# Performance work log

Hardware: AMD Instinct MI355X
Metric: run time of the kernel (lower is better)

Reference implementation:

```python
import jax, jax.numpy as jnp
import numpy as np

N, E, IN, H, C, T = 50000, 800000, 128, 64, 64, 2
F1, FO1 = H, H // T   # conv1: per-tower in/out feats
F2, FO2 = H, C // T   # conv2
STD_EPS = 1e-5
BN_EPS = 1e-5


def setup_inputs() -> dict:
    key = jax.random.key(0)
    ks = jax.random.split(key, 12)
    rn = lambda k, s, sc=0.05: jax.random.normal(k, s, jnp.float32) * sc
    return {
        "x": jax.random.normal(ks[0], (N, IN), jnp.float32),
        "embed_W": rn(ks[1], (IN, H)),
        "embed_b": jnp.zeros((H,), jnp.float32),
        "pre_W1": rn(ks[2], (T, 2 * F1, F1)),
        "pre_b1": jnp.zeros((T, F1), jnp.float32),
        "post_W1": rn(ks[3], (T, 13 * F1, FO1)),
        "post_b1": jnp.zeros((T, FO1), jnp.float32),
        "lin_W1": rn(ks[4], (H, H)),
        "lin_b1": jnp.zeros((H,), jnp.float32),
        "bn_gamma": jnp.ones((H,), jnp.float32),
        "bn_beta": jnp.zeros((H,), jnp.float32),
        "pre_W2": rn(ks[5], (T, 2 * F2, F2)),
        "pre_b2": jnp.zeros((T, F2), jnp.float32),
        "post_W2": rn(ks[6], (T, 13 * F2, FO2)),
        "post_b2": jnp.zeros((T, FO2), jnp.float32),
        "lin_W2": rn(ks[7], (C, C)),
        "lin_b2": jnp.zeros((C,), jnp.float32),
        "src": jax.random.randint(ks[8], (E,), 0, N, jnp.int32),
        "dst": jax.random.randint(ks[9], (E,), 0, N, jnp.int32),
    }


def _pna_conv(h, src, dst, deg_raw, degc, avg_log, preW, preb, postW, postb, linW, linb):
    # h: [N, F] node feats; messages flow src -> dst, aggregated at dst.
    m = jnp.concatenate([h[dst], h[src]], axis=-1)            # [E, 2F]  (cat[x_i, x_j])
    m = jnp.einsum('ef,tfg->etg', m, preW) + preb[None]       # [E, T, F] per-tower pre-NN
    seg = lambda v: jax.ops.segment_sum(v, dst, num_segments=N)
    cnt = degc[:, None, None]                                 # clamped degree >= 1
    has = (deg_raw > 0)[:, None, None]
    mean = seg(m) / cnt                                       # [N, T, F]
    mean_sq = seg(m * m) / cnt
    mn = jnp.where(has, jax.ops.segment_min(m, dst, num_segments=N), 0.0)
    mx = jnp.where(has, jax.ops.segment_max(m, dst, num_segments=N), 0.0)
    std = jnp.sqrt(jax.nn.relu(mean_sq - mean * mean) + STD_EPS)
    agg = jnp.concatenate([mean, mn, mx, std], axis=-1)       # [N, T, 4F]
    ld = jnp.log(degc + 1.0)[:, None, None]
    out = jnp.concatenate([agg, agg * (ld / avg_log), agg * (avg_log / ld)], axis=-1)  # [N, T, 12F]
    F = h.shape[-1]
    out = jnp.concatenate([jnp.broadcast_to(h[:, None, :], (N, T, F)), out], axis=-1)  # [N, T, 13F]
    out = jnp.einsum('ntf,tfg->ntg', out, postW) + postb[None]  # [N, T, FO] per-tower post-NN
    return out.reshape(N, -1) @ linW + linb                    # final mixing Linear(out, out)


def reference(x, embed_W, embed_b, pre_W1, pre_b1, post_W1, post_b1, lin_W1, lin_b1,
              bn_gamma, bn_beta, pre_W2, pre_b2, post_W2, post_b2, lin_W2, lin_b2,
              src, dst):
    deg_raw = jax.ops.segment_sum(jnp.ones((E,), jnp.float32), dst, num_segments=N)
    degc = jnp.maximum(deg_raw, 1.0)
    avg_log = jnp.mean(jnp.log(deg_raw + 1.0))  # avg_deg['log'] from the graph's degrees
    h = x @ embed_W + embed_b
    h = _pna_conv(h, src, dst, deg_raw, degc, avg_log,
                  pre_W1, pre_b1, post_W1, post_b1, lin_W1, lin_b1)
    mu = jnp.mean(h, axis=0)
    var = jnp.mean((h - mu) ** 2, axis=0)
    h = bn_gamma * (h - mu) / jnp.sqrt(var + BN_EPS) + bn_beta
    h = jax.nn.relu(h)  # dropout is identity in eval mode
    return _pna_conv(h, src, dst, deg_raw, degc, avg_log,
                     pre_W2, pre_b2, post_W2, post_b2, lin_W2, lin_b2)
```

## Files before the change

kernel.cpp:

```cpp
#include <hip/hip_runtime.h>
#include <hip/hip_fp16.h>

#define N_NODES 50000
#define E_EDGES 800000
#define IN_F    128
#define H_F     64
#define STD_EPS 1e-5f
#define BN_EPS  1e-5f

#define HIST_BLK 3125
#define EMB_BLK  768
#define SCAN_BLK 49
#define TRANS_BLK 448

typedef __attribute__((ext_vector_type(8))) short bf16x8;
typedef __attribute__((ext_vector_type(4))) float f32x4;

__device__ __forceinline__ unsigned bf16_rne(float f) {
  unsigned u = __float_as_uint(f);
  return (u + 0x7fffu + ((u >> 16) & 1u)) >> 16;
}
__device__ __forceinline__ void bf16_split2(float x, float y, unsigned& hi, unsigned& lo) {
  unsigned hx = bf16_rne(x), hy = bf16_rne(y);
  float rx = x - __uint_as_float(hx << 16);
  float ry = y - __uint_as_float(hy << 16);
  hi = hx | (hy << 16);
  lo = bf16_rne(rx) | (bf16_rne(ry) << 16);
}

#define MFMA(acc, a, b) acc = __builtin_amdgcn_mfma_f32_16x16x32_bf16(a, b, acc, 0, 0, 0)

__global__ __launch_bounds__(256) void k_hist_embed(const int* __restrict__ dst,
                                                    int* __restrict__ deg,
                                                    const float* __restrict__ x,
                                                    const float* __restrict__ W,
                                                    const float* __restrict__ bias,
                                                    float* __restrict__ h) {
  __shared__ float sW[IN_F * 64];
  __shared__ float sx[IN_F * 36];
  if (blockIdx.x < HIST_BLK) {
    int e = blockIdx.x * 256 + threadIdx.x;
    atomicAdd(&deg[dst[e]], 1);
    return;
  }
  for (int i = threadIdx.x; i < IN_F * 64; i += 256) sW[i] = W[i];
  int f = threadIdx.x & 63, ng = threadIdx.x >> 6;
  float bj = bias[f];
  const int NGRP = (N_NODES + 31) / 32;
  for (int grp = blockIdx.x - HIST_BLK; grp < NGRP; grp += EMB_BLK) {
    int n0 = grp * 32;
    __syncthreads();
    for (int idx = threadIdx.x; idx < 32 * IN_F; idx += 256) {
      int nl = idx >> 7, k = idx & 127;
      int n = n0 + nl;
      sx[k * 36 + nl] = (n < N_NODES) ? x[(size_t)n * IN_F + k] : 0.f;
    }
    __syncthreads();
    float a[8] = {bj, bj, bj, bj, bj, bj, bj, bj};
    const float* xp = &sx[ng * 8];
#pragma unroll 4
    for (int k = 0; k < IN_F; k++) {
      float4 h0 = *(const float4*)&xp[k * 36];
      float4 h1 = *(const float4*)&xp[k * 36 + 4];
      float w = sW[k * 64 + f];
      a[0] = fmaf(h0.x, w, a[0]); a[1] = fmaf(h0.y, w, a[1]);
      a[2] = fmaf(h0.z, w, a[2]); a[3] = fmaf(h0.w, w, a[3]);
      a[4] = fmaf(h1.x, w, a[4]); a[5] = fmaf(h1.y, w, a[5]);
      a[6] = fmaf(h1.z, w, a[6]); a[7] = fmaf(h1.w, w, a[7]);
    }
#pragma unroll
    for (int j = 0; j < 8; j++) {
      int n = n0 + ng * 8 + j;
      if (n < N_NODES) h[(size_t)n * 64 + f] = a[j];
    }
  }
}

__global__ __launch_bounds__(256) void k_scanpart_trans(const int* __restrict__ deg,
                                                        int* __restrict__ partials,
                                                        float* __restrict__ scalars,
                                                        const float* __restrict__ pW1,
                                                        const float* __restrict__ pW2,
                                                        const float* __restrict__ lW1,
                                                        const float* __restrict__ lW2,
                                                        unsigned short* __restrict__ WBhi,
                                                        unsigned short* __restrict__ WBlo,
                                                        float* __restrict__ lWT) {
  __shared__ int red[256];
  __shared__ float redf[256];
  if (blockIdx.x < SCAN_BLK) {
    int base = blockIdx.x * 1024;
    int s = 0; float ls = 0.f;
    for (int j = threadIdx.x; j < 1024; j += 256) {
      int i = base + j;
      if (i < N_NODES) { int d = deg[i]; s += d; ls += logf((float)d + 1.0f); }
    }
    red[threadIdx.x] = s; redf[threadIdx.x] = ls; __syncthreads();
    for (int st = 128; st > 0; st >>= 1) {
      if (threadIdx.x < st) {
        red[threadIdx.x] += red[threadIdx.x + st];
        redf[threadIdx.x] += redf[threadIdx.x + st];
      }
      __syncthreads();
    }
    if (threadIdx.x == 0) {
      partials[blockIdx.x] = red[0];
      atomicAdd(&scalars[0], redf[0]);
    }
    return;
  }
  int idx = (blockIdx.x - SCAN_BLK) * 256 + threadIdx.x;
  if (idx < 106496) {
    int f = idx % 832;
    int rest = idx / 832;
    int col = rest & 31, tt = rest >> 5;
    const float* srcp = (tt >= 2) ? pW2 : pW1;
    float v = srcp[((size_t)(tt & 1) * 832 + f) * 32 + col];
    unsigned hb = bf16_rne(v);
    float rsd = v - __uint_as_float(hb << 16);
    WBhi[idx] = (unsigned short)hb;
    WBlo[idx] = (unsigned short)bf16_rne(rsd);
  } else if (idx < 114688) {
    int jj = idx - 106496;
    int layer = jj / 4096, r2 = jj % 4096;
    int c4 = r2 / 256, r3 = r2 % 256;
    int col = r3 / 4, j = r3 % 4;
    const float* srcl = layer ? lW2 : lW1;
    lWT[jj] = srcl[(c4 * 4 + j) * 64 + col];
  }
}

__global__ __launch_bounds__(256) void k_scan_final(const int* __restrict__ deg,
                                                    const int* __restrict__ partials,
                                                    int* __restrict__ row_ptr,
                                                    int* __restrict__ cursor,
                                                    float* __restrict__ scalars) {
  __shared__ int ts[256];
  __shared__ int sbase;
  if (threadIdx.x == 0) {
    int pre = 0;
    for (int b = 0; b < (int)blockIdx.x; b++) pre += partials[b];
    sbase = pre;
    if (blockIdx.x == 0) {
      scalars[1] = scalars[0] / (float)N_NODES;
      row_ptr[N_NODES] = E_EDGES;
    }
  }
  int base = blockIdx.x * 1024 + threadIdx.x * 4;
  int d[4]; int s = 0;
#pragma unroll
  for (int j = 0; j < 4; j++) {
    int i = base + j;
    d[j] = (i < N_NODES) ? deg[i] : 0;
    s += d[j];
  }
  ts[threadIdx.x] = s; __syncthreads();
  for (int off = 1; off < 256; off <<= 1) {
    int t = (threadIdx.x >= off) ? ts[threadIdx.x - off] : 0;
    __syncthreads();
    ts[threadIdx.x] += t;
    __syncthreads();
  }
  int excl = (threadIdx.x > 0) ? ts[threadIdx.x - 1] : 0;
  int run = sbase + excl;
#pragma unroll
  for (int j = 0; j < 4; j++) {
    int i = base + j;
    if (i < N_NODES) { row_ptr[i] = run; cursor[i] = run; run += d[j]; }
  }
}

__global__ __launch_bounds__(256) void k_scatter(const int* __restrict__ src,
                                                 const int* __restrict__ dst,
                                                 int* __restrict__ cursor,
                                                 int* __restrict__ csr_src) {
  int e = blockIdx.x * 256 + threadIdx.x;
  if (e < E_EDGES) {
    int d = dst[e];
    int p = atomicAdd(&cursor[d], 1);
    csr_src[p] = src[e];
  }
}

template <bool BN>
__global__ __launch_bounds__(256) void k_preab(const float* __restrict__ hin,
                                               const float* __restrict__ preW,
                                               const float* __restrict__ preb,
                                               const float* __restrict__ bnsum,
                                               const float* __restrict__ bnsumsq,
                                               const float* __restrict__ gamma,
                                               const float* __restrict__ beta,
                                               float* __restrict__ h2out,
                                               float* __restrict__ hA,
                                               __half* __restrict__ hB) {
  __shared__ float sWp[64 * 128];
  __shared__ float sh[64 * 68];
  __shared__ float sbn[128];
  int t = blockIdx.x & 1;
  const float* Wsrc = preW + (size_t)t * 128 * 64;
  for (int i = threadIdx.x; i < 64 * 64; i += 256) {
    int k = i >> 6, f = i & 63;
    float wa = Wsrc[k * 64 + f];
    float wb = Wsrc[(64 + k) * 64 + f];
    *(float2*)&sWp[k * 128 + f * 2] = make_float2(wa, wb);
  }
  if (BN && threadIdx.x < 64) {
    int c = threadIdx.x;
    float mu = bnsum[c] * (1.f / N_NODES);
    float var = bnsumsq[c] * (1.f / N_NODES) - mu * mu;
    float sc = gamma[c] / sqrtf(var + BN_EPS);
    sbn[c] = sc;
    sbn[64 + c] = fmaf(-mu, sc, beta[c]);
  }
  int f = threadIdx.x & 63, ng = threadIdx.x >> 6;
  float pb = preb[t * 64 + f];
  int nblk2 = gridDim.x >> 1;
  const int NGRP = (N_NODES + 63) / 64;
  for (int grp = blockIdx.x >> 1; grp < NGRP; grp += nblk2) {
    int n0 = grp * 64;
    __syncthreads();
    for (int idx = threadIdx.x; idx < 64 * 64; idx += 256) {
      int nl = idx >> 6, k = idx & 63;
      int n = n0 + nl;
      float v = 0.f;
      if (n < N_NODES) {
        v = hin[(size_t)n * 64 + k];
        if (BN) {
          v = fmaxf(fmaf(v, sbn[k], sbn[64 + k]), 0.f);
          if (t == 0) h2out[(size_t)n * 64 + k] = v;
        }
      }
      sh[k * 68 + nl] = v;
    }
    __syncthreads();
    float a[16], b[16];
#pragma unroll
    for (int j = 0; j < 16; j++) { a[j] = pb; b[j] = 0.f; }
    const float* hp = &sh[ng * 16];
    const float* wp = &sWp[f * 2];
#pragma unroll 2
    for (int k = 0; k < 64; k++) {
      float4 h0 = *(const float4*)&hp[k * 68];
      float4 h1 = *(const float4*)&hp[k * 68 + 4];
      float4 h2 = *(const float4*)&hp[k * 68 + 8];
      float4 h3 = *(const float4*)&hp[k * 68 + 12];
      float2 w2 = *(const float2*)&wp[k * 128];
      a[0]  = fmaf(h0.x, w2.x, a[0]);  b[0]  = fmaf(h0.x, w2.y, b[0]);
      a[1]  = fmaf(h0.y, w2.x, a[1]);  b[1]  = fmaf(h0.y, w2.y, b[1]);
      a[2]  = fmaf(h0.z, w2.x, a[2]);  b[2]  = fmaf(h0.z, w2.y, b[2]);
      a[3]  = fmaf(h0.w, w2.x, a[3]);  b[3]  = fmaf(h0.w, w2.y, b[3]);
      a[4]  = fmaf(h1.x, w2.x, a[4]);  b[4]  = fmaf(h1.x, w2.y, b[4]);
      a[5]  = fmaf(h1.y, w2.x, a[5]);  b[5]  = fmaf(h1.y, w2.y, b[5]);
      a[6]  = fmaf(h1.z, w2.x, a[6]);  b[6]  = fmaf(h1.z, w2.y, b[6]);
      a[7]  = fmaf(h1.w, w2.x, a[7]);  b[7]  = fmaf(h1.w, w2.y, b[7]);
      a[8]  = fmaf(h2.x, w2.x, a[8]);  b[8]  = fmaf(h2.x, w2.y, b[8]);
      a[9]  = fmaf(h2.y, w2.x, a[9]);  b[9]  = fmaf(h2.y, w2.y, b[9]);
      a[10] = fmaf(h2.z, w2.x, a[10]); b[10] = fmaf(h2.z, w2.y, b[10]);
      a[11] = fmaf(h2.w, w2.x, a[11]); b[11] = fmaf(h2.w, w2.y, b[11]);
      a[12] = fmaf(h3.x, w2.x, a[12]); b[12] = fmaf(h3.x, w2.y, b[12]);
      a[13] = fmaf(h3.y, w2.x, a[13]); b[13] = fmaf(h3.y, w2.y, b[13]);
      a[14] = fmaf(h3.z, w2.x, a[14]); b[14] = fmaf(h3.z, w2.y, b[14]);
      a[15] = fmaf(h3.w, w2.x, a[15]); b[15] = fmaf(h3.w, w2.y, b[15]);
    }
    int tf = t * 64 + f;
#pragma unroll
    for (int j = 0; j < 16; j++) {
      int n = n0 + ng * 16 + j;
      if (n < N_NODES) {
        hA[(size_t)n * 128 + tf] = a[j];
        hB[(size_t)n * 128 + tf] = __float2half(b[j]);
      }
    }
  }
}

__global__ __launch_bounds__(256, 8) void k_conv(const float* __restrict__ hA,
                                                 const __half* __restrict__ hB,
                                                 const float* __restrict__ hskip,
                                                 const int* __restrict__ row_ptr,
                                                 const int* __restrict__ csr_src,
                                                 const unsigned short* __restrict__ WBhi,
                                                 const unsigned short* __restrict__ WBlo,
                                                 const float* __restrict__ postb,
                                                 const float* __restrict__ linWT,
                                                 const float* __restrict__ linb,
                                                 const float* __restrict__ scalars,
                                                 float* __restrict__ out) {
  __shared__ unsigned sAhi[2560];
  __shared__ unsigned sAlo[2560];
  int w = threadIdx.x >> 6, lane = threadIdx.x & 63;
  int n0 = blockIdx.x * 8;
  int t = lane >> 5, fb2 = (lane & 31) * 2;
  int off = t * 64 + fb2;
  float avg = scalars[1];

#pragma unroll 1
  for (int k = 0; k < 2; k++) {
    int nl = w * 2 + k;
    int n = n0 + nl;
    float2 a = *(const float2*)&hA[(size_t)n * 128 + off];
    float2 hsv = *(const float2*)&hskip[(size_t)n * 64 + fb2];
    int rp0 = __builtin_amdgcn_readfirstlane(row_ptr[n]);
    int rp1 = __builtin_amdgcn_readfirstlane(row_ptr[n + 1]);
    int dg = rp1 - rp0;
    float sx0=0,sy0=0,qx0=0,qy0=0, sx1=0,sy1=0,qx1=0,qy1=0;
    float mnx0=INFINITY,mny0=INFINITY,mxx0=-INFINITY,mxy0=-INFINITY;
    float mnx1=INFINITY,mny1=INFINITY,mxx1=-INFINITY,mxy1=-INFINITY;
    int nloop = dg >> 3;
    if (nloop > 0) {
      int b = rp0;
      int s0=csr_src[b],s1=csr_src[b+1],s2=csr_src[b+2],s3=csr_src[b+3],
          s4=csr_src[b+4],s5=csr_src[b+5],s6=csr_src[b+6],s7=csr_src[b+7];
      __half2 qa0 = *(const __half2*)&hB[(size_t)s0 * 128 + off];
      __half2 qa1 = *(const __half2*)&hB[(size_t)s1 * 128 + off];
      __half2 qa2 = *(const __half2*)&hB[(size_t)s2 * 128 + off];
      __half2 qa3 = *(const __half2*)&hB[(size_t)s3 * 128 + off];
      __half2 qa4 = *(const __half2*)&hB[(size_t)s4 * 128 + off];
      __half2 qa5 = *(const __half2*)&hB[(size_t)s5 * 128 + off];
      __half2 qa6 = *(const __half2*)&hB[(size_t)s6 * 128 + off];
      __half2 qa7 = *(const __half2*)&hB[(size_t)s7 * 128 + off];
      for (int it = 0; ; it++) {
        bool more = (it + 1 < nloop);
        __half2 qb0, qb1, qb2, qb3, qb4, qb5, qb6, qb7;
        if (more) {
          int c = rp0 + ((it + 1) << 3);
          s0=csr_src[c];s1=csr_src[c+1];s2=csr_src[c+2];s3=csr_src[c+3];
          s4=csr_src[c+4];s5=csr_src[c+5];s6=csr_src[c+6];s7=csr_src[c+7];
          qb0 = *(const __half2*)&hB[(size_t)s0 * 128 + off];
          qb1 = *(const __half2*)&hB[(size_t)s1 * 128 + off];
          qb2 = *(const __half2*)&hB[(size_t)s2 * 128 + off];
          qb3 = *(const __half2*)&hB[(size_t)s3 * 128 + off];
          qb4 = *(const __half2*)&hB[(size_t)s4 * 128 + off];
          qb5 = *(const __half2*)&hB[(size_t)s5 * 128 + off];
          qb6 = *(const __half2*)&hB[(size_t)s6 * 128 + off];
          qb7 = *(const __half2*)&hB[(size_t)s7 * 128 + off];
        }
        float2 v0 = __half22float2(qa0), v1 = __half22float2(qa1);
        float2 v2 = __half22float2(qa2), v3 = __half22float2(qa3);
        float2 v4 = __half22float2(qa4), v5 = __half22float2(qa5);
        float2 v6 = __half22float2(qa6), v7 = __half22float2(qa7);
        sx0 += v0.x; qx0 = fmaf(v0.x,v0.x,qx0); mnx0 = fminf(mnx0,v0.x); mxx0 = fmaxf(mxx0,v0.x);
        sy0 += v0.y; qy0 = fmaf(v0.y,v0.y,qy0); mny0 = fminf(mny0,v0.y); mxy0 = fmaxf(mxy0,v0.y);
        sx1 += v1.x; qx1 = fmaf(v1.x,v1.x,qx1); mnx1 = fminf(mnx1,v1.x); mxx1 = fmaxf(mxx1,v1.x);
        sy1 += v1.y; qy1 = fmaf(v1.y,v1.y,qy1); mny1 = fminf(mny1,v1.y); mxy1 = fmaxf(mxy1,v1.y);
        sx0 += v2.x; qx0 = fmaf(v2.x,v2.x,qx0); mnx0 = fminf(mnx0,v2.x); mxx0 = fmaxf(mxx0,v2.x);
        sy0 += v2.y; qy0 = fmaf(v2.y,v2.y,qy0); mny0 = fminf(mny0,v2.y); mxy0 = fmaxf(mxy0,v2.y);
        sx1 += v3.x; qx1 = fmaf(v3.x,v3.x,qx1); mnx1 = fminf(mnx1,v3.x); mxx1 = fmaxf(mxx1,v3.x);
        sy1 += v3.y; qy1 = fmaf(v3.y,v3.y,qy1); mny1 = fminf(mny1,v3.y); mxy1 = fmaxf(mxy1,v3.y);
        sx0 += v4.x; qx0 = fmaf(v4.x,v4.x,qx0); mnx0 = fminf(mnx0,v4.x); mxx0 = fmaxf(mxx0,v4.x);
        sy0 += v4.y; qy0 = fmaf(v4.y,v4.y,qy0); mny0 = fminf(mny0,v4.y); mxy0 = fmaxf(mxy0,v4.y);
        sx1 += v5.x; qx1 = fmaf(v5.x,v5.x,qx1); mnx1 = fminf(mnx1,v5.x); mxx1 = fmaxf(mxx1,v5.x);
        sy1 += v5.y; qy1 = fmaf(v5.y,v5.y,qy1); mny1 = fminf(mny1,v5.y); mxy1 = fmaxf(mxy1,v5.y);
        sx0 += v6.x; qx0 = fmaf(v6.x,v6.x,qx0); mnx0 = fminf(mnx0,v6.x); mxx0 = fmaxf(mxx0,v6.x);
        sy0 += v6.y; qy0 = fmaf(v6.y,v6.y,qy0); mny0 = fminf(mny0,v6.y); mxy0 = fmaxf(mxy0,v6.y);
        sx1 += v7.x; qx1 = fmaf(v7.x,v7.x,qx1); mnx1 = fminf(mnx1,v7.x); mxx1 = fmaxf(mxx1,v7.x);
        sy1 += v7.y; qy1 = fmaf(v7.y,v7.y,qy1); mny1 = fminf(mny1,v7.y); mxy1 = fmaxf(mxy1,v7.y);
        if (!more) break;
        qa0=qb0; qa1=qb1; qa2=qb2; qa3=qb3; qa4=qb4; qa5=qb5; qa6=qb6; qa7=qb7;
      }
    }
    {
      int i = rp0 + (nloop << 3);
      int r = rp1 - i;
      if (r > 0) {
        int sj[7];
#pragma unroll
        for (int j = 0; j < 7; j++) sj[j] = csr_src[i + (j < r ? j : r - 1)];
        __half2 hq[7];
#pragma unroll
        for (int j = 0; j < 7; j++) hq[j] = *(const __half2*)&hB[(size_t)sj[j] * 128 + off];
#pragma unroll
        for (int j = 0; j < 7; j++) {
          if (j < r) {
            float2 v = __half22float2(hq[j]);
            if (j & 1) {
              sx1 += v.x; qx1 = fmaf(v.x,v.x,qx1); mnx1 = fminf(mnx1,v.x); mxx1 = fmaxf(mxx1,v.x);
              sy1 += v.y; qy1 = fmaf(v.y,v.y,qy1); mny1 = fminf(mny1,v.y); mxy1 = fmaxf(mxy1,v.y);
            } else {
              sx0 += v.x; qx0 = fmaf(v.x,v.x,qx0); mnx0 = fminf(mnx0,v.x); mxx0 = fmaxf(mxx0,v.x);
              sy0 += v.y; qy0 = fmaf(v.y,v.y,qy0); mny0 = fminf(mny0,v.y); mxy0 = fmaxf(mxy0,v.y);
            }
          }
        }
      }
    }
    float cnt = (float)(dg > 0 ? dg : 1);
    float inv = 1.0f / cnt;
    float mrx = (sx0 + sx1) * inv, mry = (sy0 + sy1) * inv;
    float sdx = sqrtf(fmaxf((qx0 + qx1) * inv - mrx * mrx, 0.f) + STD_EPS);
    float sdy = sqrtf(fmaxf((qy0 + qy1) * inv - mry * mry, 0.f) + STD_EPS);
    float mnx = fminf(mnx0, mnx1), mny = fminf(mny0, mny1);
    float mxx = fmaxf(mxx0, mxx1), mxy = fmaxf(mxy0, mxy1);
    float ax = a.x, ay = a.y;
    if (dg == 0) { mnx = 0; mny = 0; mxx = 0; mxy = 0; ax = 0; ay = 0; }
    float meanx = mrx + ax, meany = mry + ay;
    mnx += ax; mny += ay; mxx += ax; mxy += ay;
    unsigned* ahp = &sAhi[(t * 8 + nl) * 160];
    unsigned* alp = &sAlo[(t * 8 + nl) * 160];
    int sw = (nl & 3) << 2;
    int p = lane & 31;
    unsigned hi, lo;
    bf16_split2(hsv.x, hsv.y, hi, lo);   ahp[p ^ sw]         = hi; alp[p ^ sw]         = lo;
    bf16_split2(meanx, meany, hi, lo);   ahp[(p + 32) ^ sw]  = hi; alp[(p + 32) ^ sw]  = lo;
    bf16_split2(mnx, mny, hi, lo);       ahp[(p + 64) ^ sw]  = hi; alp[(p + 64) ^ sw]  = lo;
    bf16_split2(mxx, mxy, hi, lo);       ahp[(p + 96) ^ sw]  = hi; alp[(p + 96) ^ sw]  = lo;
    bf16_split2(sdx, sdy, hi, lo);       ahp[(p + 128) ^ sw] = hi; alp[(p + 128) ^ sw] = lo;
  }
  __syncthreads();

  f32x4 acc1 = {0.f, 0.f, 0.f, 0.f};
  f32x4 acc2 = {0.f, 0.f, 0.f, 0.f};
  f32x4 acc3 = {0.f, 0.f, 0.f, 0.f};
  int tw = w >> 1, ntile = w & 1;
  int kq = lane >> 4;
  {
    const bf16x8* Ah = (const bf16x8*)(sAhi + (tw * 8 + (lane & 7)) * 160);
    const bf16x8* Al = (const bf16x8*)(sAlo + (tw * 8 + (lane & 7)) * 160);
    int kqs = kq ^ (lane & 3);
    int brow = (tw * 32 + ntile * 16 + (lane & 15)) * 104 + kq;
    const bf16x8* Bh = (const bf16x8*)WBhi + brow;
    const bf16x8* Bl = (const bf16x8*)WBlo + brow;
    bf16x8 bh_0 = Bh[0], bl_0 = Bl[0];
    bf16x8 bh_1 = Bh[4], bl_1 = Bl[4];
#pragma unroll
    for (int s = 0; s < 10; s++) {
      bf16x8 bh_n, bl_n;
      if (s < 8) { bh_n = Bh[(s + 2) * 4]; bl_n = Bl[(s + 2) * 4]; }
      bf16x8 ah = Ah[s * 4 + kqs], al = Al[s * 4 + kqs];
      MFMA(acc1, ah, bh_0); MFMA(acc1, al, bh_0); MFMA(acc1, ah, bl_0);
      bh_0 = bh_1; bl_0 = bl_1; bh_1 = bh_n; bl_1 = bl_n;
    }
    bf16x8 c_0 = Bh[40], d_0 = Bh[72];
    bf16x8 c_1 = Bh[44], d_1 = Bh[76];
#pragma unroll
    for (int s = 0; s < 8; s++) {
      bf16x8 c_n, d_n;
      if (s < 6) { c_n = Bh[48 + s * 4]; d_n = Bh[80 + s * 4]; }
      bf16x8 ah = Ah[(s + 2) * 4 + kqs], al = Al[(s + 2) * 4 + kqs];
      MFMA(acc2, ah, c_0); MFMA(acc2, al, c_0);
      MFMA(acc3, ah, d_0); MFMA(acc3, al, d_0);
      c_0 = c_1; d_0 = d_1; c_1 = c_n; d_1 = d_n;
    }
  }
  __syncthreads();

  float* spo = (float*)sAhi;
  if (lane < 32) {
    int colg = tw * 32 + ntile * 16 + (lane & 15);
    float pbv = postb[colg];
    int rbase = kq * 4;
    int rb = n0 + rbase;
    int p0 = row_ptr[rb], p1 = row_ptr[rb+1], p2 = row_ptr[rb+2],
        p3 = row_ptr[rb+3], p4 = row_ptr[rb+4];
    int dgv[4] = {p1 - p0, p2 - p1, p3 - p2, p4 - p3};
#pragma unroll
    for (int r = 0; r < 4; r++) {
      float cnt = (float)(dgv[r] > 0 ? dgv[r] : 1);
      float ldv = logf(cnt + 1.f);
      spo[(rbase + r) * 64 + colg] =
          acc1[r] + (ldv / avg) * acc2[r] + (avg / ldv) * acc3[r] + pbv;
    }
  }
  __syncthreads();

  {
    float la0 = linb[lane], la1 = la0;
    const float4* lw4 = (const float4*)linWT + lane;
    const float* p0 = &spo[(w * 2) * 64];
    const float* p1 = p0 + 64;
#pragma unroll
    for (int c4 = 0; c4 < 16; c4++) {
      float4 lwv = lw4[c4 * 64];
      float4 pa = *(const float4*)&p0[c4 * 4];
      float4 pb2 = *(const float4*)&p1[c4 * 4];
      la0 = fmaf(pa.w, lwv.w, fmaf(pa.z, lwv.z, fmaf(pa.y, lwv.y, fmaf(pa.x, lwv.x, la0))));
      la1 = fmaf(pb2.w, lwv.w, fmaf(pb2.z, lwv.z, fmaf(pb2.y, lwv.y, fmaf(pb2.x, lwv.x, la1))));
    }
    size_t ob = (size_t)(n0 + w * 2) * 64 + lane;
    out[ob] = la0;
    out[ob + 64] = la1;
  }
}

__global__ __launch_bounds__(256) void k_bnstats(const float* __restrict__ y,
                                                 float* __restrict__ bnsum,
                                                 float* __restrict__ bnsumsq) {
  __shared__ float r1[256], r2[256];
  int c = threadIdx.x & 63, r = threadIdx.x >> 6;
  float s = 0, q = 0;
  for (int n = blockIdx.x * 4 + r; n < N_NODES; n += gridDim.x * 4) {
    float v = y[(size_t)n * 64 + c];
    s += v; q = fmaf(v, v, q);
  }
  r1[threadIdx.x] = s; r2[threadIdx.x] = q; __syncthreads();
  if (threadIdx.x < 64) {
    s = r1[threadIdx.x] + r1[threadIdx.x + 64] + r1[threadIdx.x + 128] + r1[threadIdx.x + 192];
    q = r2[threadIdx.x] + r2[threadIdx.x + 64] + r2[threadIdx.x + 128] + r2[threadIdx.x + 192];
    atomicAdd(&bnsum[threadIdx.x], s);
    atomicAdd(&bnsumsq[threadIdx.x], q);
  }
}

extern "C" void kernel_launch(void* const* d_in, const int* in_sizes, int n_in,
                              void* d_out, int out_size, void* d_ws, size_t ws_size,
                              hipStream_t stream) {
  const float* x      = (const float*)d_in[0];
  const float* embW   = (const float*)d_in[1];
  const float* embB   = (const float*)d_in[2];
  const float* preW1  = (const float*)d_in[3];
  const float* preb1  = (const float*)d_in[4];
  const float* postW1 = (const float*)d_in[5];
  const float* postb1 = (const float*)d_in[6];
  const float* linW1  = (const float*)d_in[7];
  const float* linb1  = (const float*)d_in[8];
  const float* gamma  = (const float*)d_in[9];
  const float* beta   = (const float*)d_in[10];
  const float* preW2  = (const float*)d_in[11];
  const float* preb2  = (const float*)d_in[12];
  const float* postW2 = (const float*)d_in[13];
  const float* postb2 = (const float*)d_in[14];
  const float* linW2  = (const float*)d_in[15];
  const float* linb2  = (const float*)d_in[16];
  const int*   src    = (const int*)d_in[17];
  const int*   dst    = (const int*)d_in[18];
  float* out = (float*)d_out;

  char* w = (char*)d_ws;
  size_t o = 0;
  int*   deg     = (int*)(w + o);   o += (size_t)N_NODES * 4;
  float* scalars = (float*)(w + o); o += 64;
  float* bnsum   = (float*)(w + o); o += 256;
  float* bnsumsq = (float*)(w + o); o += 256;
  size_t zero_len = o;
  o = (o + 255) & ~(size_t)255;
  int* partials = (int*)(w + o);  o += 256;
  int* row_ptr  = (int*)(w + o);  o += (size_t)(N_NODES + 1) * 4; o = (o + 255) & ~(size_t)255;
  int* cursor   = (int*)(w + o);  o += (size_t)N_NODES * 4;       o = (o + 255) & ~(size_t)255;
  int* csr      = (int*)(w + o);  o += (size_t)E_EDGES * 4;       o = (o + 255) & ~(size_t)255;
  unsigned short* WBhi = (unsigned short*)(w + o); o += (size_t)2 * 53248 * 2;
  unsigned short* WBlo = (unsigned short*)(w + o); o += (size_t)2 * 53248 * 2;
  float* linWT  = (float*)(w + o); o += (size_t)2 * 4096 * 4;
  float* h1 = (float*)(w + o); o += (size_t)N_NODES * 64 * 4;
  float* y1 = (float*)(w + o); o += (size_t)N_NODES * 64 * 4;
  float* h2 = (float*)(w + o); o += (size_t)N_NODES * 64 * 4;
  float* hA = (float*)(w + o); o += (size_t)N_NODES * 128 * 4;
  __half* hBh = (__half*)(w + o); o += (size_t)N_NODES * 128 * 2;

  hipMemsetAsync(w, 0, zero_len, stream);

  k_hist_embed<<<HIST_BLK + EMB_BLK, 256, 0, stream>>>(dst, deg, x, embW, embB, h1);
  k_scanpart_trans<<<SCAN_BLK + TRANS_BLK, 256, 0, stream>>>(
      deg, partials, scalars, postW1, postW2, linW1, linW2, WBhi, WBlo, linWT);
  k_scan_final<<<SCAN_BLK, 256, 0, stream>>>(deg, partials, row_ptr, cursor, scalars);
  k_scatter<<<(E_EDGES + 255) / 256, 256, 0, stream>>>(src, dst, cursor, csr);

  k_preab<false><<<768, 256, 0, stream>>>(h1, preW1, preb1, nullptr, nullptr,
                                          nullptr, nullptr, nullptr, hA, hBh);
  k_conv<<<N_NODES / 8, 256, 0, stream>>>(hA, hBh, h1, row_ptr, csr,
                                          WBhi, WBlo, postb1, linWT, linb1, scalars, y1);
  k_bnstats<<<256, 256, 0, stream>>>(y1, bnsum, bnsumsq);
  k_preab<true><<<768, 256, 0, stream>>>(y1, preW2, preb2, bnsum, bnsumsq,
                                         gamma, beta, h2, hA, hBh);
  k_conv<<<N_NODES / 8, 256, 0, stream>>>(hA, hBh, h2, row_ptr, csr,
                                          WBhi + 53248, WBlo + 53248, postb2,
                                          linWT + 4096, linb2, scalars, out);
}
```

Measured before the change: 574.9 us.

## Interleave gather loops for two nodes per wave with padded 8-edge batches

Each wave now gathers neighbours for both of its nodes together, with double-buffered 8-edge batches for each node, instead of processing the two nodes one after the other. The tail is handled by clamping indices and masking, so the separate remainder path is gone. Edge indices are made wave-uniform with readfirstlane, and the LDS swizzle is widened from 4 to 8 rows to cut bank conflicts. The cost is more registers, so launch bounds drop from 8 to 6 blocks per CU, and padded batches issue redundant loads.

```diff
diff --git a/kernel.cpp b/kernel.cpp
--- a/kernel.cpp
+++ b/kernel.cpp
@@ -274,7 +274,65 @@
   }
 }
 
-__global__ __launch_bounds__(256, 8) void k_conv(const float* __restrict__ hA,
+#define GATHER8(D0,D1,D2,D3,D4,D5,D6,D7, bb, rl)                              \
+  { int _s0 = __builtin_amdgcn_readfirstlane(csr_src[min((bb)+0,(rl))]);      \
+    int _s1 = __builtin_amdgcn_readfirstlane(csr_src[min((bb)+1,(rl))]);      \
+    int _s2 = __builtin_amdgcn_readfirstlane(csr_src[min((bb)+2,(rl))]);      \
+    int _s3 = __builtin_amdgcn_readfirstlane(csr_src[min((bb)+3,(rl))]);      \
+    int _s4 = __builtin_amdgcn_readfirstlane(csr_src[min((bb)+4,(rl))]);      \
+    int _s5 = __builtin_amdgcn_readfirstlane(csr_src[min((bb)+5,(rl))]);      \
+    int _s6 = __builtin_amdgcn_readfirstlane(csr_src[min((bb)+6,(rl))]);      \
+    int _s7 = __builtin_amdgcn_readfirstlane(csr_src[min((bb)+7,(rl))]);      \
+    D0 = hB2[((size_t)_s0 << 6) + oh2];                                       \
+    D1 = hB2[((size_t)_s1 << 6) + oh2];                                       \
+    D2 = hB2[((size_t)_s2 << 6) + oh2];                                       \
+    D3 = hB2[((size_t)_s3 << 6) + oh2];                                       \
+    D4 = hB2[((size_t)_s4 << 6) + oh2];                                       \
+    D5 = hB2[((size_t)_s5 << 6) + oh2];                                       \
+    D6 = hB2[((size_t)_s6 << 6) + oh2];                                       \
+    D7 = hB2[((size_t)_s7 << 6) + oh2]; }
+
+#define EDGE1(vv, P, S)                                                       \
+  { float2 _f = __half22float2(vv);                                           \
+    P##sx##S += _f.x; P##qx##S = fmaf(_f.x, _f.x, P##qx##S);                  \
+    P##mnx##S = fminf(P##mnx##S, _f.x); P##mxx##S = fmaxf(P##mxx##S, _f.x);   \
+    P##sy##S += _f.y; P##qy##S = fmaf(_f.y, _f.y, P##qy##S);                  \
+    P##mny##S = fminf(P##mny##S, _f.y); P##mxy##S = fmaxf(P##mxy##S, _f.y); }
+
+#define COMP8(A0,A1,A2,A3,A4,A5,A6,A7, m8, dg, P)                             \
+  { if ((m8)+0 < (dg)) EDGE1(A0, P, 0);                                       \
+    if ((m8)+1 < (dg)) EDGE1(A1, P, 1);                                       \
+    if ((m8)+2 < (dg)) EDGE1(A2, P, 0);                                       \
+    if ((m8)+3 < (dg)) EDGE1(A3, P, 1);                                       \
+    if ((m8)+4 < (dg)) EDGE1(A4, P, 0);                                       \
+    if ((m8)+5 < (dg)) EDGE1(A5, P, 1);                                       \
+    if ((m8)+6 < (dg)) EDGE1(A6, P, 0);                                       \
+    if ((m8)+7 < (dg)) EDGE1(A7, P, 1); }
+
+#define FINALIZE(P, dg, a, hs, nl)                                            \
+  { float cnt = (float)((dg) > 0 ? (dg) : 1);                                 \
+    float inv = 1.0f / cnt;                                                   \
+    float mrx = (P##sx0 + P##sx1) * inv, mry = (P##sy0 + P##sy1) * inv;       \
+    float sdx = sqrtf(fmaxf((P##qx0 + P##qx1) * inv - mrx * mrx, 0.f) + STD_EPS); \
+    float sdy = sqrtf(fmaxf((P##qy0 + P##qy1) * inv - mry * mry, 0.f) + STD_EPS); \
+    float mnx = fminf(P##mnx0, P##mnx1), mny = fminf(P##mny0, P##mny1);       \
+    float mxx = fmaxf(P##mxx0, P##mxx1), mxy = fmaxf(P##mxy0, P##mxy1);       \
+    float ax = (a).x, ay = (a).y;                                             \
+    if ((dg) == 0) { mnx = 0; mny = 0; mxx = 0; mxy = 0; ax = 0; ay = 0; }    \
+    float meanx = mrx + ax, meany = mry + ay;                                 \
+    mnx += ax; mny += ay; mxx += ax; mxy += ay;                               \
+    unsigned* ahp = &sAhi[(t * 8 + (nl)) * 160];                              \
+    unsigned* alp = &sAlo[(t * 8 + (nl)) * 160];                              \
+    int sw = ((nl) & 7) << 2;                                                 \
+    int p = lane & 31;                                                        \
+    unsigned hi, lo;                                                          \
+    bf16_split2((hs).x, (hs).y, hi, lo); ahp[p ^ sw] = hi; alp[p ^ sw] = lo;  \
+    bf16_split2(meanx, meany, hi, lo); ahp[(p+32) ^ sw] = hi; alp[(p+32) ^ sw] = lo; \
+    bf16_split2(mnx, mny, hi, lo);     ahp[(p+64) ^ sw] = hi; alp[(p+64) ^ sw] = lo; \
+    bf16_split2(mxx, mxy, hi, lo);     ahp[(p+96) ^ sw] = hi; alp[(p+96) ^ sw] = lo; \
+    bf16_split2(sdx, sdy, hi, lo);     ahp[(p+128) ^ sw] = hi; alp[(p+128) ^ sw] = lo; }
+
+__global__ __launch_bounds__(256, 6) void k_conv(const float* __restrict__ hA,
                                                  const __half* __restrict__ hB,
                                                  const float* __restrict__ hskip,
                                                  const int* __restrict__ row_ptr,
@@ -294,118 +352,50 @@
   int off = t * 64 + fb2;
   float avg = scalars[1];
 
+  const __half2* hB2 = (const __half2*)hB;
+  int oh2 = (t << 5) | (lane & 31);
+
+  int nu = n0 + w * 2;
+  float2 au = *(const float2*)&hA[(size_t)nu * 128 + off];
+  float2 av = *(const float2*)&hA[(size_t)(nu + 1) * 128 + off];
+  float2 hsu = *(const float2*)&hskip[(size_t)nu * 64 + fb2];
+  float2 hsv = *(const float2*)&hskip[(size_t)(nu + 1) * 64 + fb2];
+  int rpu0 = __builtin_amdgcn_readfirstlane(row_ptr[nu]);
+  int rpu1 = __builtin_amdgcn_readfirstlane(row_ptr[nu + 1]);
+  int rpv1 = __builtin_amdgcn_readfirstlane(row_ptr[nu + 2]);
+  int dgu = rpu1 - rpu0, dgv = rpv1 - rpu1;
+  int rlu = rpu1 - 1, rlv = rpv1 - 1;
+  int nbu = (dgu + 7) >> 3, nbv = (dgv + 7) >> 3;
+  int M = nbu > nbv ? nbu : nbv;
+
+  float usx0=0,uqx0=0,usy0=0,uqy0=0, usx1=0,uqx1=0,usy1=0,uqy1=0;
+  float umnx0=INFINITY,umny0=INFINITY,umxx0=-INFINITY,umxy0=-INFINITY;
+  float umnx1=INFINITY,umny1=INFINITY,umxx1=-INFINITY,umxy1=-INFINITY;
+  float vsx0=0,vqx0=0,vsy0=0,vqy0=0, vsx1=0,vqx1=0,vsy1=0,vqy1=0;
+  float vmnx0=INFINITY,vmny0=INFINITY,vmxx0=-INFINITY,vmxy0=-INFINITY;
+  float vmnx1=INFINITY,vmny1=INFINITY,vmxx1=-INFINITY,vmxy1=-INFINITY;
+
+  __half2 UA0{},UA1{},UA2{},UA3{},UA4{},UA5{},UA6{},UA7{};
+  __half2 UB0{},UB1{},UB2{},UB3{},UB4{},UB5{},UB6{},UB7{};
+  __half2 VA0{},VA1{},VA2{},VA3{},VA4{},VA5{},VA6{},VA7{};
+  __half2 VB0{},VB1{},VB2{},VB3{},VB4{},VB5{},VB6{},VB7{};
+
+  if (nbu > 0) GATHER8(UA0,UA1,UA2,UA3,UA4,UA5,UA6,UA7, rpu0, rlu);
+  if (nbv > 0) GATHER8(VA0,VA1,VA2,VA3,VA4,VA5,VA6,VA7, rpu1, rlv);
 #pragma unroll 1
-  for (int k = 0; k < 2; k++) {
-    int nl = w * 2 + k;
-    int n = n0 + nl;
-    float2 a = *(const float2*)&hA[(size_t)n * 128 + off];
-    float2 hsv = *(const float2*)&hskip[(size_t)n * 64 + fb2];
-    int rp0 = __builtin_amdgcn_readfirstlane(row_ptr[n]);
-    int rp1 = __builtin_amdgcn_readfirstlane(row_ptr[n + 1]);
-    int dg = rp1 - rp0;
-    float sx0=0,sy0=0,qx0=0,qy0=0, sx1=0,sy1=0,qx1=0,qy1=0;
-    float mnx0=INFINITY,mny0=INFINITY,mxx0=-INFINITY,mxy0=-INFINITY;
-    float mnx1=INFINITY,mny1=INFINITY,mxx1=-INFINITY,mxy1=-INFINITY;
-    int nloop = dg >> 3;
-    if (nloop > 0) {
-      int b = rp0;
-      int s0=csr_src[b],s1=csr_src[b+1],s2=csr_src[b+2],s3=csr_src[b+3],
-          s4=csr_src[b+4],s5=csr_src[b+5],s6=csr_src[b+6],s7=csr_src[b+7];
-      __half2 qa0 = *(const __half2*)&hB[(size_t)s0 * 128 + off];
-      __half2 qa1 = *(const __half2*)&hB[(size_t)s1 * 128 + off];
-      __half2 qa2 = *(const __half2*)&hB[(size_t)s2 * 128 + off];
-      __half2 qa3 = *(const __half2*)&hB[(size_t)s3 * 128 + off];
-      __half2 qa4 = *(const __half2*)&hB[(size_t)s4 * 128 + off];
-      __half2 qa5 = *(const __half2*)&hB[(size_t)s5 * 128 + off];
-      __half2 qa6 = *(const __half2*)&hB[(size_t)s6 * 128 + off];
-      __half2 qa7 = *(const __half2*)&hB[(size_t)s7 * 128 + off];
-      for (int it = 0; ; it++) {
-        bool more = (it + 1 < nloop);
-        __half2 qb0, qb1, qb2, qb3, qb4, qb5, qb6, qb7;
-        if (more) {
-          int c = rp0 + ((it + 1) << 3);
-          s0=csr_src[c];s1=csr_src[c+1];s2=csr_src[c+2];s3=csr_src[c+3];
-          s4=csr_src[c+4];s5=csr_src[c+5];s6=csr_src[c+6];s7=csr_src[c+7];
-          qb0 = *(const __half2*)&hB[(size_t)s0 * 128 + off];
-          qb1 = *(const __half2*)&hB[(size_t)s1 * 128 + off];
-          qb2 = *(const __half2*)&hB[(size_t)s2 * 128 + off];
-          qb3 = *(const __half2*)&hB[(size_t)s3 * 128 + off];
-          qb4 = *(const __half2*)&hB[(size_t)s4 * 128 + off];
-          qb5 = *(const __half2*)&hB[(size_t)s5 * 128 + off];
-          qb6 = *(const __half2*)&hB[(size_t)s6 * 128 + off];
-          qb7 = *(const __half2*)&hB[(size_t)s7 * 128 + off];
-        }
-        float2 v0 = __half22float2(qa0), v1 = __half22float2(qa1);
-        float2 v2 = __half22float2(qa2), v3 = __half22float2(qa3);
-        float2 v4 = __half22float2(qa4), v5 = __half22float2(qa5);
-        float2 v6 = __half22float2(qa6), v7 = __half22float2(qa7);
-        sx0 += v0.x; qx0 = fmaf(v0.x,v0.x,qx0); mnx0 = fminf(mnx0,v0.x); mxx0 = fmaxf(mxx0,v0.x);
-        sy0 += v0.y; qy0 = fmaf(v0.y,v0.y,qy0); mny0 = fminf(mny0,v0.y); mxy0 = fmaxf(mxy0,v0.y);
-        sx1 += v1.x; qx1 = fmaf(v1.x,v1.x,qx1); mnx1 = fminf(mnx1,v1.x); mxx1 = fmaxf(mxx1,v1.x);
-        sy1 += v1.y; qy1 = fmaf(v1.y,v1.y,qy1); mny1 = fminf(mny1,v1.y); mxy1 = fmaxf(mxy1,v1.y);
-        sx0 += v2.x; qx0 = fmaf(v2.x,v2.x,qx0); mnx0 = fminf(mnx0,v2.x); mxx0 = fmaxf(mxx0,v2.x);
-        sy0 += v2.y; qy0 = fmaf(v2.y,v2.y,qy0); mny0 = fminf(mny0,v2.y); mxy0 = fmaxf(mxy0,v2.y);
-        sx1 += v3.x; qx1 = fmaf(v3.x,v3.x,qx1); mnx1 = fminf(mnx1,v3.x); mxx1 = fmaxf(mxx1,v3.x);
-        sy1 += v3.y; qy1 = fmaf(v3.y,v3.y,qy1); mny1 = fminf(mny1,v3.y); mxy1 = fmaxf(mxy1,v3.y);
-        sx0 += v4.x; qx0 = fmaf(v4.x,v4.x,qx0); mnx0 = fminf(mnx0,v4.x); mxx0 = fmaxf(mxx0,v4.x);
-        sy0 += v4.y; qy0 = fmaf(v4.y,v4.y,qy0); mny0 = fminf(mny0,v4.y); mxy0 = fmaxf(mxy0,v4.y);
-        sx1 += v5.x; qx1 = fmaf(v5.x,v5.x,qx1); mnx1 = fminf(mnx1,v5.x); mxx1 = fmaxf(mxx1,v5.x);
-        sy1 += v5.y; qy1 = fmaf(v5.y,v5.y,qy1); mny1 = fminf(mny1,v5.y); mxy1 = fmaxf(mxy1,v5.y);
-        sx0 += v6.x; qx0 = fmaf(v6.x,v6.x,qx0); mnx0 = fminf(mnx0,v6.x); mxx0 = fmaxf(mxx0,v6.x);
-        sy0 += v6.y; qy0 = fmaf(v6.y,v6.y,qy0); mny0 = fminf(mny0,v6.y); mxy0 = fmaxf(mxy0,v6.y);
-        sx1 += v7.x; qx1 = fmaf(v7.x,v7.x,qx1); mnx1 = fminf(mnx1,v7.x); mxx1 = fmaxf(mxx1,v7.x);
-        sy1 += v7.y; qy1 = fmaf(v7.y,v7.y,qy1); mny1 = fminf(mny1,v7.y); mxy1 = fmaxf(mxy1,v7.y);
-        if (!more) break;
-        qa0=qb0; qa1=qb1; qa2=qb2; qa3=qb3; qa4=qb4; qa5=qb5; qa6=qb6; qa7=qb7;
-      }
-    }
-    {
-      int i = rp0 + (nloop << 3);
-      int r = rp1 - i;
-      if (r > 0) {
-        int sj[7];
-#pragma unroll
-        for (int j = 0; j < 7; j++) sj[j] = csr_src[i + (j < r ? j : r - 1)];
-        __half2 hq[7];
-#pragma unroll
-        for (int j = 0; j < 7; j++) hq[j] = *(const __half2*)&hB[(size_t)sj[j] * 128 + off];
-#pragma unroll
-        for (int j = 0; j < 7; j++) {
-          if (j < r) {
-            float2 v = __half22float2(hq[j]);
-            if (j & 1) {
-              sx1 += v.x; qx1 = fmaf(v.x,v.x,qx1); mnx1 = fminf(mnx1,v.x); mxx1 = fmaxf(mxx1,v.x);
-              sy1 += v.y; qy1 = fmaf(v.y,v.y,qy1); mny1 = fminf(mny1,v.y); mxy1 = fmaxf(mxy1,v.y);
-            } else {
-              sx0 += v.x; qx0 = fmaf(v.x,v.x,qx0); mnx0 = fminf(mnx0,v.x); mxx0 = fmaxf(mxx0,v.x);
-              sy0 += v.y; qy0 = fmaf(v.y,v.y,qy0); mny0 = fminf(mny0,v.y); mxy0 = fmaxf(mxy0,v.y);
-            }
-          }
-        }
-      }
-    }
-    float cnt = (float)(dg > 0 ? dg : 1);
-    float inv = 1.0f / cnt;
-    float mrx = (sx0 + sx1) * inv, mry = (sy0 + sy1) * inv;
-    float sdx = sqrtf(fmaxf((qx0 + qx1) * inv - mrx * mrx, 0.f) + STD_EPS);
-    float sdy = sqrtf(fmaxf((qy0 + qy1) * inv - mry * mry, 0.f) + STD_EPS);
-    float mnx = fminf(mnx0, mnx1), mny = fminf(mny0, mny1);
-    float mxx = fmaxf(mxx0, mxx1), mxy = fmaxf(mxy0, mxy1);
-    float ax = a.x, ay = a.y;
-    if (dg == 0) { mnx = 0; mny = 0; mxx = 0; mxy = 0; ax = 0; ay = 0; }
-    float meanx = mrx + ax, meany = mry + ay;
-    mnx += ax; mny += ay; mxx += ax; mxy += ay;
-    unsigned* ahp = &sAhi[(t * 8 + nl) * 160];
-    unsigned* alp = &sAlo[(t * 8 + nl) * 160];
-    int sw = (nl & 3) << 2;
-    int p = lane & 31;
-    unsigned hi, lo;
-    bf16_split2(hsv.x, hsv.y, hi, lo);   ahp[p ^ sw]         = hi; alp[p ^ sw]         = lo;
-    bf16_split2(meanx, meany, hi, lo);   ahp[(p + 32) ^ sw]  = hi; alp[(p + 32) ^ sw]  = lo;
-    bf16_split2(mnx, mny, hi, lo);       ahp[(p + 64) ^ sw]  = hi; alp[(p + 64) ^ sw]  = lo;
-    bf16_split2(mxx, mxy, hi, lo);       ahp[(p + 96) ^ sw]  = hi; alp[(p + 96) ^ sw]  = lo;
-    bf16_split2(sdx, sdy, hi, lo);       ahp[(p + 128) ^ sw] = hi; alp[(p + 128) ^ sw] = lo;
-  }
+  for (int m = 0; m < M; m++) {
+    int bu = rpu0 + m * 8 + 8, bv = rpu1 + m * 8 + 8;
+    if (m + 1 < nbu) GATHER8(UB0,UB1,UB2,UB3,UB4,UB5,UB6,UB7, bu, rlu);
+    if (m + 1 < nbv) GATHER8(VB0,VB1,VB2,VB3,VB4,VB5,VB6,VB7, bv, rlv);
+    int m8 = m << 3;
+    if (m < nbu) COMP8(UA0,UA1,UA2,UA3,UA4,UA5,UA6,UA7, m8, dgu, u);
+    if (m < nbv) COMP8(VA0,VA1,VA2,VA3,VA4,VA5,VA6,VA7, m8, dgv, v);
+    UA0=UB0;UA1=UB1;UA2=UB2;UA3=UB3;UA4=UB4;UA5=UB5;UA6=UB6;UA7=UB7;
+    VA0=VB0;VA1=VB1;VA2=VB2;VA3=VB3;VA4=VB4;VA5=VB5;VA6=VB6;VA7=VB7;
+  }
+
+  FINALIZE(u, dgu, au, hsu, w * 2);
+  FINALIZE(v, dgv, av, hsv, w * 2 + 1);
   __syncthreads();
 
   f32x4 acc1 = {0.f, 0.f, 0.f, 0.f};
@@ -413,10 +403,10 @@
   f32x4 acc3 = {0.f, 0.f, 0.f, 0.f};
   int tw = w >> 1, ntile = w & 1;
   int kq = lane >> 4;
+  int rsw = lane & 7;
   {
     const bf16x8* Ah = (const bf16x8*)(sAhi + (tw * 8 + (lane & 7)) * 160);
     const bf16x8* Al = (const bf16x8*)(sAlo + (tw * 8 + (lane & 7)) * 160);
-    int kqs = kq ^ (lane & 3);
     int brow = (tw * 32 + ntile * 16 + (lane & 15)) * 104 + kq;
     const bf16x8* Bh = (const bf16x8*)WBhi + brow;
     const bf16x8* Bl = (const bf16x8*)WBlo + brow;
@@ -426,7 +416,7 @@
     for (int s = 0; s < 10; s++) {
       bf16x8 bh_n, bl_n;
       if (s < 8) { bh_n = Bh[(s + 2) * 4]; bl_n = Bl[(s + 2) * 4]; }
-      bf16x8 ah = Ah[s * 4 + kqs], al = Al[s * 4 + kqs];
+      bf16x8 ah = Ah[(s * 4 + kq) ^ rsw], al = Al[(s * 4 + kq) ^ rsw];
       MFMA(acc1, ah, bh_0); MFMA(acc1, al, bh_0); MFMA(acc1, ah, bl_0);
       bh_0 = bh_1; bl_0 = bl_1; bh_1 = bh_n; bl_1 = bl_n;
     }
@@ -436,7 +426,7 @@
     for (int s = 0; s < 8; s++) {
       bf16x8 c_n, d_n;
       if (s < 6) { c_n = Bh[48 + s * 4]; d_n = Bh[80 + s * 4]; }
-      bf16x8 ah = Ah[(s + 2) * 4 + kqs], al = Al[(s + 2) * 4 + kqs];
+      bf16x8 ah = Ah[((s + 2) * 4 + kq) ^ rsw], al = Al[((s + 2) * 4 + kq) ^ rsw];
       MFMA(acc2, ah, c_0); MFMA(acc2, al, c_0);
       MFMA(acc3, ah, d_0); MFMA(acc3, al, d_0);
       c_0 = c_1; d_0 = d_1; c_1 = c_n; d_1 = d_n;
@@ -452,10 +442,10 @@
     int rb = n0 + rbase;
     int p0 = row_ptr[rb], p1 = row_ptr[rb+1], p2 = row_ptr[rb+2],
         p3 = row_ptr[rb+3], p4 = row_ptr[rb+4];
-    int dgv[4] = {p1 - p0, p2 - p1, p3 - p2, p4 - p3};
+    int dgv4[4] = {p1 - p0, p2 - p1, p3 - p2, p4 - p3};
 #pragma unroll
     for (int r = 0; r < 4; r++) {
-      float cnt = (float)(dgv[r] > 0 ? dgv[r] : 1);
+      float cnt = (float)(dgv4[r] > 0 ? dgv4[r] : 1);
       float ldv = logf(cnt + 1.f);
       spo[(rbase + r) * 64 + colg] =
           acc1[r] + (ldv / avg) * acc2[r] + (avg / ldv) * acc3[r] + pbv;
```

Measured after the change: 570.4 us. About the same (-0.8%).
